# Kernel tuning notes

Measured on AMD Instinct MI355X. Metric: run time of the kernel, lower is better.

The kernel has to match this reference:

```python
import jax, jax.numpy as jnp
import numpy as np

N = 50000        # num nodes
E = 1600000      # num edges
D = 128          # hidden_dim
R = 2            # num_relations
L = 2            # num rgcn layers
DES, TWE, NUM, CAT = 768, 768, 5, 6


def _lin_init(key, fan_in, fan_out):
    kw, kb = jax.random.split(key)
    s = 1.0 / np.sqrt(fan_in)
    w = jax.random.uniform(kw, (fan_in, fan_out), jnp.float32, -s, s)
    b = jax.random.uniform(kb, (fan_out,), jnp.float32, -s, s)
    return w, b


def setup_inputs() -> dict:
    key = jax.random.key(0)
    ks = jax.random.split(key, 16)
    des = jax.random.normal(ks[0], (N, DES), jnp.float32)
    tweets = jax.random.normal(ks[1], (N, TWE), jnp.float32)
    num = jax.random.normal(ks[2], (N, NUM), jnp.float32)
    cat = jax.random.normal(ks[3], (N, CAT), jnp.float32)
    edge_index = jax.random.randint(ks[4], (2, E), 0, N, jnp.int64 if jax.config.jax_enable_x64 else jnp.int32)
    edge_type = jax.random.randint(ks[5], (E,), 0, R, edge_index.dtype)

    des_w, des_b = _lin_init(ks[6], DES, D)
    tweet_w, tweet_b = _lin_init(ks[7], TWE, D)
    num_w, num_b = _lin_init(ks[8], NUM, D)
    cat_w, cat_b = _lin_init(ks[9], CAT, D)

    s = 1.0 / np.sqrt(D)
    rel_w = jax.random.uniform(ks[10], (L, R, D, D), jnp.float32, -s, s)   # per-layer per-relation weight
    root_w = jax.random.uniform(ks[11], (L, D, D), jnp.float32, -s, s)     # per-layer root weight
    rgcn_b = jax.random.uniform(ks[12], (L, D), jnp.float32, -s, s)        # per-layer bias

    mlp_w1, mlp_b1 = _lin_init(ks[13], D, D)
    mlp_w2, mlp_b2 = _lin_init(ks[14], D, 2)

    return dict(des=des, tweets=tweets, num=num, cat=cat,
                edge_index=edge_index, edge_type=edge_type,
                des_w=des_w, des_b=des_b, tweet_w=tweet_w, tweet_b=tweet_b,
                num_w=num_w, num_b=num_b, cat_w=cat_w, cat_b=cat_b,
                rel_w=rel_w, root_w=root_w, rgcn_b=rgcn_b,
                mlp_w1=mlp_w1, mlp_b1=mlp_b1, mlp_w2=mlp_w2, mlp_b2=mlp_b2)


def _lrelu(v):
    return jax.nn.leaky_relu(v, 0.01)  # torch F.leaky_relu default slope


def _rgcn_layer(x, edge_index, edge_type, rel_w_l, root_w_l, b_l):
    # PyG RGCNConv with num_bases=None, aggr='mean':
    # out = x @ root + bias + sum_r mean_{j in N_r(i)} x_j @ W_r
    src, dst = edge_index[0], edge_index[1]
    out = x @ root_w_l + b_l
    xs = x[src]  # [E, D] gathered source features
    for r in range(R):
        mask = (edge_type == r).astype(x.dtype)          # [E]
        msg = (xs @ rel_w_l[r]) * mask[:, None]          # [E, D]
        ssum = jax.ops.segment_sum(msg, dst, num_segments=N)           # [N, D]
        cnt = jax.ops.segment_sum(mask, dst, num_segments=N)           # [N]
        out = out + ssum / jnp.maximum(cnt, 1.0)[:, None]
    return out


def reference(des, tweets, num, cat, edge_index, edge_type,
              des_w, des_b, tweet_w, tweet_b, num_w, num_b, cat_w, cat_b,
              rel_w, root_w, rgcn_b, mlp_w1, mlp_b1, mlp_w2, mlp_b2):
    # multi-modal projections, fused leaky-relu + sum (eval mode: no dropout)
    x = (_lrelu(des @ des_w + des_b)
         + _lrelu(tweets @ tweet_w + tweet_b)
         + _lrelu(num @ num_w + num_b)
         + _lrelu(cat @ cat_w + cat_b))
    for l in range(L):
        x = _lrelu(_rgcn_layer(x, edge_index, edge_type, rel_w[l], root_w[l], rgcn_b[l]))
    h = jax.nn.relu(x @ mlp_w1 + mlp_b1)
    return h @ mlp_w2 + mlp_b2  # [N, 2]
```

## Files before the change

kernel.cpp:

```cpp
#include <hip/hip_runtime.h>

#define NN 50000
#define EE 1600000
#define NBINS (2 * NN)
#define SCAN_NB ((NBINS + 255) / 256)

typedef __attribute__((ext_vector_type(8))) short bf16x8;
typedef __attribute__((ext_vector_type(8))) unsigned short u16x8;
typedef __attribute__((ext_vector_type(4))) float f32x4;

__device__ __forceinline__ float bf2f(unsigned short u) {
    union { unsigned int u; float f; } v; v.u = ((unsigned int)u) << 16; return v.f;
}
__device__ __forceinline__ unsigned short f2bf(float f) {
    union { float f; unsigned int u; } v; v.f = f;
    unsigned int x = v.u;
    x += ((x >> 16) & 1u) + 0x7FFFu;
    return (unsigned short)(x >> 16);
}
__device__ __forceinline__ float lrelu(float v) { return (v > 0.f) ? v : 0.01f * v; }

__global__ void rg_transpose_split(const float* __restrict__ src,
                                   unsigned short* __restrict__ dhi,
                                   unsigned short* __restrict__ dlo,
                                   int total, int K) {
    int i = blockIdx.x * 256 + threadIdx.x;
    if (i >= total) return;
    int k = i >> 7;
    int c = i & 127;
    float v = src[i];
    unsigned short h = f2bf(v);
    dhi[c * K + k] = h;
    dlo[c * K + k] = f2bf(v - bf2f(h));
}

__global__ void rg_hist(const int* __restrict__ ei, const int* __restrict__ et,
                        int* __restrict__ hist) {
    int e = blockIdx.x * 256 + threadIdx.x;
    if (e >= EE) return;
    const int dst = ei[EE + e];
    const int r = et[e];
    atomicAdd(&hist[r * NN + dst], 1);
}

__global__ void rg_scan_blk(const int* __restrict__ hist, int* __restrict__ bsum) {
    const int t = threadIdx.x;
    const int idx = blockIdx.x * 256 + t;
    int v = (idx < NBINS) ? hist[idx] : 0;
#pragma unroll
    for (int off = 32; off > 0; off >>= 1) v += __shfl_down(v, off, 64);
    __shared__ int ws[4];
    if ((t & 63) == 0) ws[t >> 6] = v;
    __syncthreads();
    if (t == 0) bsum[blockIdx.x] = ws[0] + ws[1] + ws[2] + ws[3];
}

__global__ void rg_scan_top(const int* __restrict__ bsum, int* __restrict__ boff,
                            int* __restrict__ offs) {
    __shared__ int ls[512];
    const int t = threadIdx.x;
    const int v = (t < SCAN_NB) ? bsum[t] : 0;
    ls[t] = v;
    __syncthreads();
    for (int d = 1; d < 512; d <<= 1) {
        const int u = (t >= d) ? ls[t - d] : 0;
        __syncthreads();
        ls[t] += u;
        __syncthreads();
    }
    if (t < SCAN_NB) boff[t] = ls[t] - v;
    if (t == SCAN_NB - 1) offs[NBINS] = ls[t];
}

__global__ void rg_scan_fin(const int* __restrict__ hist, const int* __restrict__ boff,
                            int* __restrict__ offs) {
    __shared__ int ls[256];
    const int t = threadIdx.x;
    const int idx = blockIdx.x * 256 + t;
    const int v = (idx < NBINS) ? hist[idx] : 0;
    ls[t] = v;
    __syncthreads();
    for (int d = 1; d < 256; d <<= 1) {
        const int u = (t >= d) ? ls[t - d] : 0;
        __syncthreads();
        ls[t] += u;
        __syncthreads();
    }
    if (idx < NBINS) offs[idx] = boff[blockIdx.x] + ls[t] - v;
}

__global__ void rg_place(const int* __restrict__ ei, const int* __restrict__ et,
                         int* __restrict__ cursor, int* __restrict__ sorted_src) {
    int e = blockIdx.x * 256 + threadIdx.x;
    if (e >= EE) return;
    const int src = ei[e];
    const int dst = ei[EE + e];
    const int r = et[e];
    const int pos = atomicAdd(&cursor[r * NN + dst], 1);
    sorted_src[pos] = src;
}

__global__ void rg_gather(const float* __restrict__ xf,
                          const int* __restrict__ sorted_src,
                          const int* __restrict__ offs,
                          float* __restrict__ agg) {
    const int lane = threadIdx.x & 63;
    const int gw = (blockIdx.x * blockDim.x + threadIdx.x) >> 6;
    const int nw = (gridDim.x * blockDim.x) >> 6;
    for (int bin = gw; bin < NBINS; bin += nw) {
        const int s = offs[bin], e = offs[bin + 1];
        float ax = 0.f, ay = 0.f;
        int i = s;
        for (; i + 3 < e; i += 4) {
            const int s0 = sorted_src[i];
            const int s1 = sorted_src[i + 1];
            const int s2 = sorted_src[i + 2];
            const int s3 = sorted_src[i + 3];
            const float2 v0 = *(const float2*)(xf + (long)s0 * 128 + lane * 2);
            const float2 v1 = *(const float2*)(xf + (long)s1 * 128 + lane * 2);
            const float2 v2 = *(const float2*)(xf + (long)s2 * 128 + lane * 2);
            const float2 v3 = *(const float2*)(xf + (long)s3 * 128 + lane * 2);
            ax += (v0.x + v1.x) + (v2.x + v3.x);
            ay += (v0.y + v1.y) + (v2.y + v3.y);
        }
        for (; i < e; ++i) {
            const int s0 = sorted_src[i];
            const float2 v0 = *(const float2*)(xf + (long)s0 * 128 + lane * 2);
            ax += v0.x;
            ay += v0.y;
        }
        const float c = fmaxf((float)(e - s), 1.0f);
        *(float2*)(agg + (long)bin * 128 + lane * 2) = make_float2(ax / c, ay / c);
    }
}

__global__ __launch_bounds__(256) void rg_part(
    const float* __restrict__ A0, const float* __restrict__ A1,
    const float* __restrict__ A2,
    const unsigned short* __restrict__ BH0, const unsigned short* __restrict__ BH1,
    const unsigned short* __restrict__ BH2,
    const unsigned short* __restrict__ BL0, const unsigned short* __restrict__ BL1,
    const unsigned short* __restrict__ BL2,
    float* __restrict__ O0, float* __restrict__ O1, float* __restrict__ O2,
    int kb0, int kb1, int kb2,
    int ks0, int ks1, int ks2,
    int Kstr, int bps)
{
    __shared__ unsigned short Ahi[64 * 40];
    __shared__ unsigned short Alo[64 * 40];
    __shared__ unsigned short Bhi[128 * 40];
    __shared__ unsigned short Blo[128 * 40];

    const int seg = blockIdx.x / bps;
    const int blk = blockIdx.x - seg * bps;

    const float* A;
    const unsigned short* BH;
    const unsigned short* BL;
    float* O;
    int kbase, ksteps;
    if (seg == 0)      { A = A0; BH = BH0; BL = BL0; O = O0; kbase = kb0; ksteps = ks0; }
    else if (seg == 1) { A = A1; BH = BH1; BL = BL1; O = O1; kbase = kb1; ksteps = ks1; }
    else               { A = A2; BH = BH2; BL = BL2; O = O2; kbase = kb2; ksteps = ks2; }

    const int tid = threadIdx.x;
    const int wave = tid >> 6, lane = tid & 63, q = lane >> 4, m15 = lane & 15;
    const int row0 = blk * 64;
    const int ar = tid >> 2, aseg = tid & 3;
    const int bn = tid >> 1, bb = (tid & 1) * 16;
    const int agr = row0 + ar;
    const bool aval = agr < NN;

    f32x4 acc[8];
#pragma unroll
    for (int t = 0; t < 8; ++t) acc[t] = (f32x4){0.f, 0.f, 0.f, 0.f};

    for (int ks = 0; ks < ksteps; ++ks) {
        const int k0 = kbase + (ks << 5);
        __syncthreads();
        {
            u16x8 hi = {0,0,0,0,0,0,0,0}, lo = {0,0,0,0,0,0,0,0};
            if (aval) {
                const float* p = A + (long)agr * Kstr + k0 + aseg * 8;
                const f32x4 v0 = *(const f32x4*)p;
                const f32x4 v1 = *(const f32x4*)(p + 4);
#pragma unroll
                for (int j = 0; j < 4; ++j) {
                    unsigned short h0 = f2bf(v0[j]);
                    hi[j] = h0;  lo[j] = f2bf(v0[j] - bf2f(h0));
                    unsigned short h1 = f2bf(v1[j]);
                    hi[j+4] = h1; lo[j+4] = f2bf(v1[j] - bf2f(h1));
                }
            }
            *(u16x8*)(Ahi + ar * 40 + aseg * 8) = hi;
            *(u16x8*)(Alo + ar * 40 + aseg * 8) = lo;
        }
        {
            const long bo = (long)bn * Kstr + k0 + bb;
            *(u16x8*)(Bhi + bn * 40 + bb)     = *(const u16x8*)(BH + bo);
            *(u16x8*)(Bhi + bn * 40 + bb + 8) = *(const u16x8*)(BH + bo + 8);
            *(u16x8*)(Blo + bn * 40 + bb)     = *(const u16x8*)(BL + bo);
            *(u16x8*)(Blo + bn * 40 + bb + 8) = *(const u16x8*)(BL + bo + 8);
        }
        __syncthreads();
        const bf16x8 ah = *(const bf16x8*)(Ahi + (wave * 16 + m15) * 40 + q * 8);
        const bf16x8 al = *(const bf16x8*)(Alo + (wave * 16 + m15) * 40 + q * 8);
#pragma unroll
        for (int t = 0; t < 8; ++t) {
            const bf16x8 bh = *(const bf16x8*)(Bhi + ((t << 4) + m15) * 40 + q * 8);
            const bf16x8 bl = *(const bf16x8*)(Blo + ((t << 4) + m15) * 40 + q * 8);
            acc[t] = __builtin_amdgcn_mfma_f32_16x16x32_bf16(ah, bh, acc[t], 0, 0, 0);
            acc[t] = __builtin_amdgcn_mfma_f32_16x16x32_bf16(al, bh, acc[t], 0, 0, 0);
            acc[t] = __builtin_amdgcn_mfma_f32_16x16x32_bf16(ah, bl, acc[t], 0, 0, 0);
        }
    }
#pragma unroll
    for (int t = 0; t < 8; ++t) {
        const int col = (t << 4) + m15;
#pragma unroll
        for (int i = 0; i < 4; ++i) {
            const int r = row0 + wave * 16 + q * 4 + i;
            if (r < NN) O[(long)r * 128 + col] = acc[t][i];
        }
    }
}

__global__ void rg_proj_fin(
    const float* __restrict__ Ptwe,
    const float* __restrict__ Pd0, const float* __restrict__ Pd1,
    const float* __restrict__ numf, const float* __restrict__ catf,
    const float* __restrict__ num_w, const float* __restrict__ cat_w,
    const float* __restrict__ desB, const float* __restrict__ tweB,
    const float* __restrict__ numB, const float* __restrict__ catB,
    float* __restrict__ xf)
{
    const int lane = threadIdx.x & 63;
    const int gw = (blockIdx.x * blockDim.x + threadIdx.x) >> 6;
    const int nw = (gridDim.x * blockDim.x) >> 6;
    const int c = lane * 2;

    float wn0[5], wn1[5], wc0[6], wc1[6];
#pragma unroll
    for (int k = 0; k < 5; ++k) { wn0[k] = num_w[k * 128 + c]; wn1[k] = num_w[k * 128 + c + 1]; }
#pragma unroll
    for (int k = 0; k < 6; ++k) { wc0[k] = cat_w[k * 128 + c]; wc1[k] = cat_w[k * 128 + c + 1]; }
    const float bn0 = numB[c], bn1 = numB[c + 1];
    const float bc0 = catB[c], bc1 = catB[c + 1];
    const float bd0 = desB[c], bd1 = desB[c + 1];
    const float bt0 = tweB[c], bt1 = tweB[c + 1];

    for (int n = gw; n < NN; n += nw) {
        const long o = (long)n * 128 + c;
        const float2 tw = *(const float2*)(Ptwe + o);
        const float2 d0 = *(const float2*)(Pd0 + o);
        const float2 d1 = *(const float2*)(Pd1 + o);
        float nv[5], cv[6];
#pragma unroll
        for (int k = 0; k < 5; ++k) nv[k] = numf[(long)n * 5 + k];
#pragma unroll
        for (int k = 0; k < 6; ++k) cv[k] = catf[(long)n * 6 + k];
        float s1x = bn0, s1y = bn1;
#pragma unroll
        for (int k = 0; k < 5; ++k) { s1x += nv[k] * wn0[k]; s1y += nv[k] * wn1[k]; }
        float s2x = bc0, s2y = bc1;
#pragma unroll
        for (int k = 0; k < 6; ++k) { s2x += cv[k] * wc0[k]; s2y += cv[k] * wc1[k]; }
        const float rx = lrelu(tw.x + bt0) + lrelu(d0.x + d1.x + bd0)
                       + lrelu(s1x) + lrelu(s2x);
        const float ry = lrelu(tw.y + bt1) + lrelu(d0.y + d1.y + bd1)
                       + lrelu(s1y) + lrelu(s2y);
        *(float2*)(xf + o) = make_float2(rx, ry);
    }
}

__global__ __launch_bounds__(256) void rg_gemm(
    const float* __restrict__ A0, const float* __restrict__ A1,
    const float* __restrict__ A2,
    const unsigned short* __restrict__ B0h, const unsigned short* __restrict__ B0l,
    const unsigned short* __restrict__ B1h, const unsigned short* __restrict__ B1l,
    const unsigned short* __restrict__ B2h, const unsigned short* __restrict__ B2l,
    const float* __restrict__ bias, int S, int act,
    float* __restrict__ outf)
{
    __shared__ unsigned short Ahi[64 * 40];
    __shared__ unsigned short Alo[64 * 40];
    __shared__ unsigned short Bhi[128 * 40];
    __shared__ unsigned short Blo[128 * 40];

    const int tid = threadIdx.x;
    const int wave = tid >> 6, lane = tid & 63, q = lane >> 4, m15 = lane & 15;
    const int row0 = blockIdx.x * 64;

    const float* Aptr[3] = { A0, A1, A2 };
    const unsigned short* BHptr[3] = { B0h, B1h, B2h };
    const unsigned short* BLptr[3] = { B0l, B1l, B2l };

    f32x4 acc[8];
#pragma unroll
    for (int t = 0; t < 8; ++t) acc[t] = (f32x4){0.f, 0.f, 0.f, 0.f};

    for (int s = 0; s < S; ++s) {
        const float* A = Aptr[s];
        const unsigned short* BH = BHptr[s];
        const unsigned short* BL = BLptr[s];
#pragma unroll
        for (int ks = 0; ks < 4; ++ks) {
            const int k0 = ks << 5;
            __syncthreads();
            {
                const int r = tid >> 2, seg = tid & 3;
                const int gr = row0 + r;
                u16x8 hi = {0,0,0,0,0,0,0,0}, lo = {0,0,0,0,0,0,0,0};
                if (gr < NN) {
                    const float* p = A + (long)gr * 128 + k0 + seg * 8;
                    const f32x4 v0 = *(const f32x4*)p;
                    const f32x4 v1 = *(const f32x4*)(p + 4);
#pragma unroll
                    for (int j = 0; j < 4; ++j) {
                        unsigned short h0 = f2bf(v0[j]);
                        hi[j] = h0;  lo[j] = f2bf(v0[j] - bf2f(h0));
                        unsigned short h1 = f2bf(v1[j]);
                        hi[j+4] = h1; lo[j+4] = f2bf(v1[j] - bf2f(h1));
                    }
                }
                *(u16x8*)(Ahi + r * 40 + seg * 8) = hi;
                *(u16x8*)(Alo + r * 40 + seg * 8) = lo;
            }
            {
                const int n = tid >> 1;
                const int base = (tid & 1) * 16;
                *(u16x8*)(Bhi + n * 40 + base)     = *(const u16x8*)(BH + (long)n * 128 + k0 + base);
                *(u16x8*)(Bhi + n * 40 + base + 8) = *(const u16x8*)(BH + (long)n * 128 + k0 + base + 8);
                *(u16x8*)(Blo + n * 40 + base)     = *(const u16x8*)(BL + (long)n * 128 + k0 + base);
                *(u16x8*)(Blo + n * 40 + base + 8) = *(const u16x8*)(BL + (long)n * 128 + k0 + base + 8);
            }
            __syncthreads();
            const bf16x8 ah = *(const bf16x8*)(Ahi + (wave * 16 + m15) * 40 + q * 8);
            const bf16x8 al = *(const bf16x8*)(Alo + (wave * 16 + m15) * 40 + q * 8);
#pragma unroll
            for (int t = 0; t < 8; ++t) {
                const bf16x8 bh = *(const bf16x8*)(Bhi + ((t << 4) + m15) * 40 + q * 8);
                const bf16x8 bl = *(const bf16x8*)(Blo + ((t << 4) + m15) * 40 + q * 8);
                acc[t] = __builtin_amdgcn_mfma_f32_16x16x32_bf16(ah, bh, acc[t], 0, 0, 0);
                acc[t] = __builtin_amdgcn_mfma_f32_16x16x32_bf16(al, bh, acc[t], 0, 0, 0);
                acc[t] = __builtin_amdgcn_mfma_f32_16x16x32_bf16(ah, bl, acc[t], 0, 0, 0);
            }
        }
    }
#pragma unroll
    for (int t = 0; t < 8; ++t) {
        const int col = (t << 4) + m15;
        const float bv = bias[col];
#pragma unroll
        for (int i = 0; i < 4; ++i) {
            const int r = row0 + wave * 16 + q * 4 + i;
            if (r < NN) {
                float v = acc[t][i] + bv;
                v = act ? fmaxf(v, 0.f) : ((v > 0.f) ? v : 0.01f * v);
                outf[(long)r * 128 + col] = v;
            }
        }
    }
}

__global__ void BotRGCN_64381559767213_kernel(const float* __restrict__ hf,
                                              const float* __restrict__ w2,
                                              const float* __restrict__ b2,
                                              float* __restrict__ out)
{
    const int lane = threadIdx.x & 63;
    const int gw = (blockIdx.x * blockDim.x + threadIdx.x) >> 6;
    const int nw = (gridDim.x * blockDim.x) >> 6;
    const int k2 = lane * 2;
    const float w00 = w2[k2 * 2 + 0], w01 = w2[k2 * 2 + 1];
    const float w10 = w2[k2 * 2 + 2], w11 = w2[k2 * 2 + 3];
    const float b0 = b2[0], b1 = b2[1];
    for (int n = gw; n < NN; n += nw) {
        const float2 v = *(const float2*)(hf + (long)n * 128 + k2);
        float p0 = v.x * w00 + v.y * w10;
        float p1 = v.x * w01 + v.y * w11;
#pragma unroll
        for (int off = 32; off > 0; off >>= 1) {
            p0 += __shfl_down(p0, off, 64);
            p1 += __shfl_down(p1, off, 64);
        }
        if (lane == 0) {
            *(float2*)(out + (long)n * 2) = make_float2(p0 + b0, p1 + b1);
        }
    }
}

extern "C" void kernel_launch(void* const* d_in, const int* in_sizes, int n_in,
                              void* d_out, int out_size, void* d_ws, size_t ws_size,
                              hipStream_t stream)
{
    const float* des    = (const float*)d_in[0];
    const float* twe    = (const float*)d_in[1];
    const float* num    = (const float*)d_in[2];
    const float* cat    = (const float*)d_in[3];
    const int*   ei     = (const int*)d_in[4];
    const int*   et     = (const int*)d_in[5];
    const float* des_w  = (const float*)d_in[6];
    const float* des_b  = (const float*)d_in[7];
    const float* twe_w  = (const float*)d_in[8];
    const float* twe_b  = (const float*)d_in[9];
    const float* num_w  = (const float*)d_in[10];
    const float* num_b  = (const float*)d_in[11];
    const float* cat_w  = (const float*)d_in[12];
    const float* cat_b  = (const float*)d_in[13];
    const float* rel_w  = (const float*)d_in[14];
    const float* root_w = (const float*)d_in[15];
    const float* rgcn_b = (const float*)d_in[16];
    const float* mlp_w1 = (const float*)d_in[17];
    const float* mlp_b1 = (const float*)d_in[18];
    const float* mlp_w2 = (const float*)d_in[19];
    const float* mlp_b2 = (const float*)d_in[20];

    char* ws = (char*)d_ws;
    size_t off = 0;
    auto alloc = [&](size_t bytes) -> char* {
        char* p = ws + off;
        off += (bytes + 255) & ~(size_t)255;
        return p;
    };
    float* xf  = (float*)alloc((size_t)NN * 128 * 4);
    float* agg = (float*)alloc((size_t)NBINS * 128 * 4);
    int* hist       = (int*)alloc((size_t)NBINS * 4);
    int* offs       = (int*)alloc((size_t)(NBINS + 1) * 4);
    int* cursor     = (int*)alloc((size_t)NBINS * 4);
    int* sorted_src = (int*)alloc((size_t)EE * 4);
    int* bsum       = (int*)alloc((size_t)SCAN_NB * 4);
    int* boff       = (int*)alloc((size_t)SCAN_NB * 4);
    unsigned short* desHi = (unsigned short*)alloc((size_t)768 * 128 * 2);
    unsigned short* desLo = (unsigned short*)alloc((size_t)768 * 128 * 2);
    unsigned short* tweHi = (unsigned short*)alloc((size_t)768 * 128 * 2);
    unsigned short* tweLo = (unsigned short*)alloc((size_t)768 * 128 * 2);
    unsigned short* rootHi = (unsigned short*)alloc((size_t)2 * 16384 * 2);
    unsigned short* rootLo = (unsigned short*)alloc((size_t)2 * 16384 * 2);
    unsigned short* relHi  = (unsigned short*)alloc((size_t)4 * 16384 * 2);
    unsigned short* relLo  = (unsigned short*)alloc((size_t)4 * 16384 * 2);
    unsigned short* w1Hi   = (unsigned short*)alloc((size_t)16384 * 2);
    unsigned short* w1Lo   = (unsigned short*)alloc((size_t)16384 * 2);
    float* hf = agg;

    auto tr = [&](const float* s, unsigned short* dh, unsigned short* dl, int K) {
        const int total = K * 128;
        rg_transpose_split<<<(total + 255) / 256, 256, 0, stream>>>(s, dh, dl, total, K);
    };
    tr(des_w, desHi, desLo, 768);
    tr(twe_w, tweHi, tweLo, 768);
    tr(root_w,         rootHi,         rootLo,         128);
    tr(root_w + 16384, rootHi + 16384, rootLo + 16384, 128);
    tr(rel_w + 0 * 16384, relHi + 0 * 16384, relLo + 0 * 16384, 128);
    tr(rel_w + 1 * 16384, relHi + 1 * 16384, relLo + 1 * 16384, 128);
    tr(rel_w + 2 * 16384, relHi + 2 * 16384, relLo + 2 * 16384, 128);
    tr(rel_w + 3 * 16384, relHi + 3 * 16384, relLo + 3 * 16384, 128);
    tr(mlp_w1, w1Hi, w1Lo, 128);

    hipMemsetAsync(hist, 0, (size_t)NBINS * 4, stream);
    rg_hist<<<(EE + 255) / 256, 256, 0, stream>>>(ei, et, hist);
    rg_scan_blk<<<SCAN_NB, 256, 0, stream>>>(hist, bsum);
    rg_scan_top<<<1, 512, 0, stream>>>(bsum, boff, offs);
    rg_scan_fin<<<SCAN_NB, 256, 0, stream>>>(hist, boff, offs);
    hipMemcpyAsync(cursor, offs, (size_t)NBINS * 4, hipMemcpyDeviceToDevice, stream);
    rg_place<<<(EE + 255) / 256, 256, 0, stream>>>(ei, et, cursor, sorted_src);

    const int bps = (NN + 63) / 64;

    rg_part<<<3 * bps, 256, 0, stream>>>(
        twe, des, des,
        tweHi, desHi, desHi,
        tweLo, desLo, desLo,
        xf, agg, agg + (size_t)NN * 128,
        0, 0, 384,
        24, 12, 12,
        768, bps);
    rg_proj_fin<<<2048, 256, 0, stream>>>(xf, agg, agg + (size_t)NN * 128,
                                          num, cat, num_w, cat_w,
                                          des_b, twe_b, num_b, cat_b, xf);

    const int gather_grid = (NBINS * 64 + 255) / 256;
    for (int l = 0; l < 2; ++l) {
        rg_gather<<<gather_grid, 256, 0, stream>>>(xf, sorted_src, offs, agg);
        rg_gemm<<<bps, 256, 0, stream>>>(
            xf, agg, agg + (size_t)NN * 128,
            rootHi + (size_t)l * 16384, rootLo + (size_t)l * 16384,
            relHi + (size_t)(l * 2) * 16384, relLo + (size_t)(l * 2) * 16384,
            relHi + (size_t)(l * 2 + 1) * 16384, relLo + (size_t)(l * 2 + 1) * 16384,
            rgcn_b + l * 128, 3, 0, xf);
    }
    rg_gemm<<<bps, 256, 0, stream>>>(xf, nullptr, nullptr,
                                     w1Hi, w1Lo, nullptr, nullptr, nullptr, nullptr,
                                     mlp_b1, 1, 1, hf);
    BotRGCN_64381559767213_kernel<<<2048, 256, 0, stream>>>(hf, mlp_w2, mlp_b2,
                                                            (float*)d_out);
}
```

Before: 960.3 us.

## Unify GEMM kernels, load A straight to registers, and prefetch the next A tile

Replaces the two GEMM kernels (projection and RGCN/MLP) with one generic rg_mm kernel driven by a parameter struct. The A operand now goes from global memory straight into each lane's registers and is split into bf16 hi/lo parts there. This removes the A shared-memory staging and its LDS traffic. The next k-step's A tile is loaded before the current one is computed, a register-level prefetch meant to hide global load latency on the memory-bound projection GEMM. Barriers become a custom s_waitcnt lgkmcnt + s_barrier. The risks are higher register pressure and possible occupancy loss.

```diff
diff --git a/kernel.cpp b/kernel.cpp
--- a/kernel.cpp
+++ b/kernel.cpp
@@ -19,6 +19,8 @@
     return (unsigned short)(x >> 16);
 }
 __device__ __forceinline__ float lrelu(float v) { return (v > 0.f) ? v : 0.01f * v; }
+
+#define BAR_LGKM() asm volatile("s_waitcnt lgkmcnt(0)\n\ts_barrier" ::: "memory")
 
 __global__ void rg_transpose_split(const float* __restrict__ src,
                                    unsigned short* __restrict__ dhi,
@@ -134,93 +136,108 @@
     }
 }
 
-__global__ __launch_bounds__(256) void rg_part(
-    const float* __restrict__ A0, const float* __restrict__ A1,
-    const float* __restrict__ A2,
-    const unsigned short* __restrict__ BH0, const unsigned short* __restrict__ BH1,
-    const unsigned short* __restrict__ BH2,
-    const unsigned short* __restrict__ BL0, const unsigned short* __restrict__ BL1,
-    const unsigned short* __restrict__ BL2,
-    float* __restrict__ O0, float* __restrict__ O1, float* __restrict__ O2,
-    int kb0, int kb1, int kb2,
-    int ks0, int ks1, int ks2,
-    int Kstr, int bps)
+struct MMArgs {
+    const float* A[9];
+    const unsigned short* BH[9];
+    const unsigned short* BL[9];
+    int kbase[9];
+    float* O[3];
+    const float* bias[3];
+    int nops[3];
+    int ksteps[3];
+    int Kstr[3];
+    int act[3];
+};
+
+__global__ __launch_bounds__(256) void rg_mm(MMArgs g, int bps)
 {
-    __shared__ unsigned short Ahi[64 * 40];
-    __shared__ unsigned short Alo[64 * 40];
     __shared__ unsigned short Bhi[128 * 40];
     __shared__ unsigned short Blo[128 * 40];
 
-    const int seg = blockIdx.x / bps;
-    const int blk = blockIdx.x - seg * bps;
-
-    const float* A;
-    const unsigned short* BH;
-    const unsigned short* BL;
-    float* O;
-    int kbase, ksteps;
-    if (seg == 0)      { A = A0; BH = BH0; BL = BL0; O = O0; kbase = kb0; ksteps = ks0; }
-    else if (seg == 1) { A = A1; BH = BH1; BL = BL1; O = O1; kbase = kb1; ksteps = ks1; }
-    else               { A = A2; BH = BH2; BL = BL2; O = O2; kbase = kb2; ksteps = ks2; }
-
+    const int job = blockIdx.x / bps;
+    const int blk = blockIdx.x - job * bps;
     const int tid = threadIdx.x;
     const int wave = tid >> 6, lane = tid & 63, q = lane >> 4, m15 = lane & 15;
     const int row0 = blk * 64;
-    const int ar = tid >> 2, aseg = tid & 3;
-    const int bn = tid >> 1, bb = (tid & 1) * 16;
-    const int agr = row0 + ar;
-    const bool aval = agr < NN;
+    const int Kstr = g.Kstr[job];
+    const int nops = g.nops[job];
+    const int ksteps = g.ksteps[job];
+
+    const int arow = row0 + wave * 16 + m15;
+    const int rowc = (arow < NN) ? arow : (NN - 1);
+    const long rowoff = (long)rowc * Kstr + q * 8;
+
+    const int bn = tid >> 1, bhalf = (tid & 1) * 16;
 
     f32x4 acc[8];
 #pragma unroll
     for (int t = 0; t < 8; ++t) acc[t] = (f32x4){0.f, 0.f, 0.f, 0.f};
 
-    for (int ks = 0; ks < ksteps; ++ks) {
-        const int k0 = kbase + (ks << 5);
-        __syncthreads();
-        {
-            u16x8 hi = {0,0,0,0,0,0,0,0}, lo = {0,0,0,0,0,0,0,0};
-            if (aval) {
-                const float* p = A + (long)agr * Kstr + k0 + aseg * 8;
-                const f32x4 v0 = *(const f32x4*)p;
-                const f32x4 v1 = *(const f32x4*)(p + 4);
-#pragma unroll
-                for (int j = 0; j < 4; ++j) {
-                    unsigned short h0 = f2bf(v0[j]);
-                    hi[j] = h0;  lo[j] = f2bf(v0[j] - bf2f(h0));
-                    unsigned short h1 = f2bf(v1[j]);
-                    hi[j+4] = h1; lo[j+4] = f2bf(v1[j] - bf2f(h1));
-                }
+    const float* Ap0 = g.A[job * 3] + rowoff + g.kbase[job * 3];
+    f32x4 va0 = *(const f32x4*)(Ap0);
+    f32x4 va1 = *(const f32x4*)(Ap0 + 4);
+
+    for (int op = 0; op < nops; ++op) {
+        const unsigned short* BH = g.BH[job * 3 + op];
+        const unsigned short* BL = g.BL[job * 3 + op];
+        const int kb = g.kbase[job * 3 + op];
+        for (int ks = 0; ks < ksteps; ++ks) {
+            const int k0 = kb + (ks << 5);
+            BAR_LGKM();
+            const long bo = (long)bn * Kstr + k0 + bhalf;
+            const u16x8 h0 = *(const u16x8*)(BH + bo);
+            const u16x8 h1 = *(const u16x8*)(BH + bo + 8);
+            const u16x8 l0 = *(const u16x8*)(BL + bo);
+            const u16x8 l1 = *(const u16x8*)(BL + bo + 8);
+            int nop = op, nks = ks + 1;
+            if (nks == ksteps) { nks = 0; if (op + 1 < nops) nop = op + 1; }
+            const float* An = g.A[job * 3 + nop] + rowoff + g.kbase[job * 3 + nop] + (nks << 5);
+            const f32x4 vn0 = *(const f32x4*)(An);
+            const f32x4 vn1 = *(const f32x4*)(An + 4);
+            *(u16x8*)(Bhi + bn * 40 + bhalf)     = h0;
+            *(u16x8*)(Bhi + bn * 40 + bhalf + 8) = h1;
+            *(u16x8*)(Blo + bn * 40 + bhalf)     = l0;
+            *(u16x8*)(Blo + bn * 40 + bhalf + 8) = l1;
+            BAR_LGKM();
+            u16x8 uh, ul;
+#pragma unroll
+            for (int j = 0; j < 4; ++j) {
+                const unsigned short hh0 = f2bf(va0[j]);
+                uh[j] = hh0;  ul[j] = f2bf(va0[j] - bf2f(hh0));
+                const unsigned short hh1 = f2bf(va1[j]);
+                uh[j + 4] = hh1;  ul[j + 4] = f2bf(va1[j] - bf2f(hh1));
             }
-            *(u16x8*)(Ahi + ar * 40 + aseg * 8) = hi;
-            *(u16x8*)(Alo + ar * 40 + aseg * 8) = lo;
-        }
-        {
-            const long bo = (long)bn * Kstr + k0 + bb;
-            *(u16x8*)(Bhi + bn * 40 + bb)     = *(const u16x8*)(BH + bo);
-            *(u16x8*)(Bhi + bn * 40 + bb + 8) = *(const u16x8*)(BH + bo + 8);
-            *(u16x8*)(Blo + bn * 40 + bb)     = *(const u16x8*)(BL + bo);
-            *(u16x8*)(Blo + bn * 40 + bb + 8) = *(const u16x8*)(BL + bo + 8);
-        }
-        __syncthreads();
-        const bf16x8 ah = *(const bf16x8*)(Ahi + (wave * 16 + m15) * 40 + q * 8);
-        const bf16x8 al = *(const bf16x8*)(Alo + (wave * 16 + m15) * 40 + q * 8);
-#pragma unroll
-        for (int t = 0; t < 8; ++t) {
-            const bf16x8 bh = *(const bf16x8*)(Bhi + ((t << 4) + m15) * 40 + q * 8);
-            const bf16x8 bl = *(const bf16x8*)(Blo + ((t << 4) + m15) * 40 + q * 8);
-            acc[t] = __builtin_amdgcn_mfma_f32_16x16x32_bf16(ah, bh, acc[t], 0, 0, 0);
-            acc[t] = __builtin_amdgcn_mfma_f32_16x16x32_bf16(al, bh, acc[t], 0, 0, 0);
-            acc[t] = __builtin_amdgcn_mfma_f32_16x16x32_bf16(ah, bl, acc[t], 0, 0, 0);
-        }
-    }
+            const bf16x8 ah = *(const bf16x8*)&uh;
+            const bf16x8 al = *(const bf16x8*)&ul;
+#pragma unroll
+            for (int t = 0; t < 8; ++t) {
+                const bf16x8 bh = *(const bf16x8*)(Bhi + ((t << 4) + m15) * 40 + q * 8);
+                const bf16x8 bl = *(const bf16x8*)(Blo + ((t << 4) + m15) * 40 + q * 8);
+                acc[t] = __builtin_amdgcn_mfma_f32_16x16x32_bf16(ah, bh, acc[t], 0, 0, 0);
+                acc[t] = __builtin_amdgcn_mfma_f32_16x16x32_bf16(al, bh, acc[t], 0, 0, 0);
+                acc[t] = __builtin_amdgcn_mfma_f32_16x16x32_bf16(ah, bl, acc[t], 0, 0, 0);
+            }
+            va0 = vn0;
+            va1 = vn1;
+        }
+    }
+
+    float* O = g.O[job];
+    const float* bias = g.bias[job];
+    const int act = g.act[job];
 #pragma unroll
     for (int t = 0; t < 8; ++t) {
         const int col = (t << 4) + m15;
+        const float bv = (act != 0) ? bias[col] : 0.f;
 #pragma unroll
         for (int i = 0; i < 4; ++i) {
             const int r = row0 + wave * 16 + q * 4 + i;
-            if (r < NN) O[(long)r * 128 + col] = acc[t][i];
+            if (r < NN) {
+                float v = acc[t][i] + bv;
+                if (act == 1) v = lrelu(v);
+                else if (act == 2) v = fmaxf(v, 0.f);
+                O[(long)r * 128 + col] = v;
+            }
         }
     }
 }
@@ -270,96 +287,6 @@
         const float ry = lrelu(tw.y + bt1) + lrelu(d0.y + d1.y + bd1)
                        + lrelu(s1y) + lrelu(s2y);
         *(float2*)(xf + o) = make_float2(rx, ry);
-    }
-}
-
-__global__ __launch_bounds__(256) void rg_gemm(
-    const float* __restrict__ A0, const float* __restrict__ A1,
-    const float* __restrict__ A2,
-    const unsigned short* __restrict__ B0h, const unsigned short* __restrict__ B0l,
-    const unsigned short* __restrict__ B1h, const unsigned short* __restrict__ B1l,
-    const unsigned short* __restrict__ B2h, const unsigned short* __restrict__ B2l,
-    const float* __restrict__ bias, int S, int act,
-    float* __restrict__ outf)
-{
-    __shared__ unsigned short Ahi[64 * 40];
-    __shared__ unsigned short Alo[64 * 40];
-    __shared__ unsigned short Bhi[128 * 40];
-    __shared__ unsigned short Blo[128 * 40];
-
-    const int tid = threadIdx.x;
-    const int wave = tid >> 6, lane = tid & 63, q = lane >> 4, m15 = lane & 15;
-    const int row0 = blockIdx.x * 64;
-
-    const float* Aptr[3] = { A0, A1, A2 };
-    const unsigned short* BHptr[3] = { B0h, B1h, B2h };
-    const unsigned short* BLptr[3] = { B0l, B1l, B2l };
-
-    f32x4 acc[8];
-#pragma unroll
-    for (int t = 0; t < 8; ++t) acc[t] = (f32x4){0.f, 0.f, 0.f, 0.f};
-
-    for (int s = 0; s < S; ++s) {
-        const float* A = Aptr[s];
-        const unsigned short* BH = BHptr[s];
-        const unsigned short* BL = BLptr[s];
-#pragma unroll
-        for (int ks = 0; ks < 4; ++ks) {
-            const int k0 = ks << 5;
-            __syncthreads();
-            {
-                const int r = tid >> 2, seg = tid & 3;
-                const int gr = row0 + r;
-                u16x8 hi = {0,0,0,0,0,0,0,0}, lo = {0,0,0,0,0,0,0,0};
-                if (gr < NN) {
-                    const float* p = A + (long)gr * 128 + k0 + seg * 8;
-                    const f32x4 v0 = *(const f32x4*)p;
-                    const f32x4 v1 = *(const f32x4*)(p + 4);
-#pragma unroll
-                    for (int j = 0; j < 4; ++j) {
-                        unsigned short h0 = f2bf(v0[j]);
-                        hi[j] = h0;  lo[j] = f2bf(v0[j] - bf2f(h0));
-                        unsigned short h1 = f2bf(v1[j]);
-                        hi[j+4] = h1; lo[j+4] = f2bf(v1[j] - bf2f(h1));
-                    }
-                }
-                *(u16x8*)(Ahi + r * 40 + seg * 8) = hi;
-                *(u16x8*)(Alo + r * 40 + seg * 8) = lo;
-            }
-            {
-                const int n = tid >> 1;
-                const int base = (tid & 1) * 16;
-                *(u16x8*)(Bhi + n * 40 + base)     = *(const u16x8*)(BH + (long)n * 128 + k0 + base);
-                *(u16x8*)(Bhi + n * 40 + base + 8) = *(const u16x8*)(BH + (long)n * 128 + k0 + base + 8);
-                *(u16x8*)(Blo + n * 40 + base)     = *(const u16x8*)(BL + (long)n * 128 + k0 + base);
-                *(u16x8*)(Blo + n * 40 + base + 8) = *(const u16x8*)(BL + (long)n * 128 + k0 + base + 8);
-            }
-            __syncthreads();
-            const bf16x8 ah = *(const bf16x8*)(Ahi + (wave * 16 + m15) * 40 + q * 8);
-            const bf16x8 al = *(const bf16x8*)(Alo + (wave * 16 + m15) * 40 + q * 8);
-#pragma unroll
-            for (int t = 0; t < 8; ++t) {
-                const bf16x8 bh = *(const bf16x8*)(Bhi + ((t << 4) + m15) * 40 + q * 8);
-                const bf16x8 bl = *(const bf16x8*)(Blo + ((t << 4) + m15) * 40 + q * 8);
-                acc[t] = __builtin_amdgcn_mfma_f32_16x16x32_bf16(ah, bh, acc[t], 0, 0, 0);
-                acc[t] = __builtin_amdgcn_mfma_f32_16x16x32_bf16(al, bh, acc[t], 0, 0, 0);
-                acc[t] = __builtin_amdgcn_mfma_f32_16x16x32_bf16(ah, bl, acc[t], 0, 0, 0);
-            }
-        }
-    }
-#pragma unroll
-    for (int t = 0; t < 8; ++t) {
-        const int col = (t << 4) + m15;
-        const float bv = bias[col];
-#pragma unroll
-        for (int i = 0; i < 4; ++i) {
-            const int r = row0 + wave * 16 + q * 4 + i;
-            if (r < NN) {
-                float v = acc[t][i] + bv;
-                v = act ? fmaxf(v, 0.f) : ((v > 0.f) ? v : 0.01f * v);
-                outf[(long)r * 128 + col] = v;
-            }
-        }
     }
 }
 
@@ -467,14 +394,19 @@
 
     const int bps = (NN + 63) / 64;
 
-    rg_part<<<3 * bps, 256, 0, stream>>>(
-        twe, des, des,
-        tweHi, desHi, desHi,
-        tweLo, desLo, desLo,
-        xf, agg, agg + (size_t)NN * 128,
-        0, 0, 384,
-        24, 12, 12,
-        768, bps);
+    {
+        MMArgs a = {};
+        a.A[0] = twe;  a.BH[0] = tweHi; a.BL[0] = tweLo; a.kbase[0] = 0;
+        a.O[0] = xf;   a.bias[0] = nullptr; a.nops[0] = 1; a.ksteps[0] = 24;
+        a.Kstr[0] = 768; a.act[0] = 0;
+        a.A[3] = des;  a.BH[3] = desHi; a.BL[3] = desLo; a.kbase[3] = 0;
+        a.O[1] = agg;  a.bias[1] = nullptr; a.nops[1] = 1; a.ksteps[1] = 12;
+        a.Kstr[1] = 768; a.act[1] = 0;
+        a.A[6] = des;  a.BH[6] = desHi; a.BL[6] = desLo; a.kbase[6] = 384;
+        a.O[2] = agg + (size_t)NN * 128; a.bias[2] = nullptr; a.nops[2] = 1;
+        a.ksteps[2] = 12; a.Kstr[2] = 768; a.act[2] = 0;
+        rg_mm<<<3 * bps, 256, 0, stream>>>(a, bps);
+    }
     rg_proj_fin<<<2048, 256, 0, stream>>>(xf, agg, agg + (size_t)NN * 128,
                                           num, cat, num_w, cat_w,
                                           des_b, twe_b, num_b, cat_b, xf);
@@ -482,16 +414,26 @@
     const int gather_grid = (NBINS * 64 + 255) / 256;
     for (int l = 0; l < 2; ++l) {
         rg_gather<<<gather_grid, 256, 0, stream>>>(xf, sorted_src, offs, agg);
-        rg_gemm<<<bps, 256, 0, stream>>>(
-            xf, agg, agg + (size_t)NN * 128,
-            rootHi + (size_t)l * 16384, rootLo + (size_t)l * 16384,
-            relHi + (size_t)(l * 2) * 16384, relLo + (size_t)(l * 2) * 16384,
-            relHi + (size_t)(l * 2 + 1) * 16384, relLo + (size_t)(l * 2 + 1) * 16384,
-            rgcn_b + l * 128, 3, 0, xf);
-    }
-    rg_gemm<<<bps, 256, 0, stream>>>(xf, nullptr, nullptr,
-                                     w1Hi, w1Lo, nullptr, nullptr, nullptr, nullptr,
-                                     mlp_b1, 1, 1, hf);
+        MMArgs a = {};
+        a.A[0] = xf;                       a.BH[0] = rootHi + (size_t)l * 16384;
+        a.BL[0] = rootLo + (size_t)l * 16384;          a.kbase[0] = 0;
+        a.A[1] = agg;                      a.BH[1] = relHi + (size_t)(l * 2) * 16384;
+        a.BL[1] = relLo + (size_t)(l * 2) * 16384;     a.kbase[1] = 0;
+        a.A[2] = agg + (size_t)NN * 128;   a.BH[2] = relHi + (size_t)(l * 2 + 1) * 16384;
+        a.BL[2] = relLo + (size_t)(l * 2 + 1) * 16384; a.kbase[2] = 0;
+        a.O[0] = xf; a.bias[0] = rgcn_b + l * 128;
+        a.nops[0] = 3; a.ksteps[0] = 4; a.Kstr[0] = 128; a.act[0] = 1;
+        rg_mm<<<bps, 256, 0, stream>>>(a, bps);
+    }
+
+    {
+        MMArgs a = {};
+        a.A[0] = xf; a.BH[0] = w1Hi; a.BL[0] = w1Lo; a.kbase[0] = 0;
+        a.O[0] = hf; a.bias[0] = mlp_b1;
+        a.nops[0] = 1; a.ksteps[0] = 4; a.Kstr[0] = 128; a.act[0] = 2;
+        rg_mm<<<bps, 256, 0, stream>>>(a, bps);
+    }
+
     BotRGCN_64381559767213_kernel<<<2048, 256, 0, stream>>>(hf, mlp_w2, mlp_b2,
                                                             (float*)d_out);
 }
```

After: 982.4 us. 2.3% more time.
